# Performance work log

Hardware: AMD Instinct MI355X
Metric: run time of the kernel (lower is better)

The kernel has to match this reference:

```python
import jax, jax.numpy as jnp
import numpy as np

H, D, HID = 16, 128, 2048
B, S = 2, 2048
NUM_BLOCKS, BLOCK_SIZE = 32, 128


def _rope(x, cos, sin):
    # x: [T, H, D]; cos/sin: [T, D/2] (neox / rotate-half style)
    half = x.shape[-1] // 2
    x1, x2 = x[..., :half], x[..., half:]
    c = cos[:, None, :]
    s = sin[:, None, :]
    return jnp.concatenate([x1 * c - x2 * s, x2 * c + x1 * s], axis=-1)


def setup_inputs() -> dict:
    key = jax.random.key(0)
    ks = jax.random.split(key, 6)
    T = B * S
    hidden_states = jax.random.normal(ks[0], (T, HID), jnp.float32)
    wqkv = jax.random.normal(ks[1], (HID, 3 * HID), jnp.float32) * 0.02
    bqkv = jax.random.normal(ks[2], (3 * HID,), jnp.float32) * 0.02
    wo = jax.random.normal(ks[3], (HID, HID), jnp.float32) * 0.02
    # rotary tables, base 10000, dim = head_size
    inv_freq = 1.0 / (10000.0 ** (jnp.arange(0, D, 2, dtype=jnp.float32) / D))  # [D/2]
    pos = jnp.tile(jnp.arange(S, dtype=jnp.float32), B)  # positions per token [T]
    ang = pos[:, None] * inv_freq[None, :]  # [T, D/2]
    cos, sin = jnp.cos(ang), jnp.sin(ang)
    k_cache = jnp.zeros((NUM_BLOCKS, BLOCK_SIZE, H, D), jnp.float32)
    v_cache = jnp.zeros((NUM_BLOCKS, BLOCK_SIZE, H, D), jnp.float32)
    cu_seqlen_prefill = jnp.array([0, S, 2 * S], jnp.int32)
    slots = jnp.arange(T, dtype=jnp.int32)
    return {"hidden_states": hidden_states, "cos": cos, "sin": sin,
            "wqkv": wqkv, "bqkv": bqkv, "wo": wo,
            "k_cache": k_cache, "v_cache": v_cache,
            "cu_seqlen_prefill": cu_seqlen_prefill, "slots": slots, "max_s": S}


def reference(hidden_states, cos, sin, wqkv, bqkv, wo, k_cache, v_cache,
              cu_seqlen_prefill, slots, max_s):
    T = hidden_states.shape[0]
    # fused QKV projection (c_attn)
    qkv = hidden_states @ wqkv + bqkv  # [T, 3*H*D]
    q, k, v = jnp.split(qkv, [H * D, 2 * H * D], axis=1)
    q = q.reshape(T, H, D)
    k = k.reshape(T, H, D)
    v = v.reshape(T, H, D)
    # rotary embedding on q and k (in-place in torch; functional here)
    q = _rope(q, cos, sin)
    k = _rope(k, cos, sin)
    # reshape_and_cache: scatter post-rope k and v into paged KV cache by slot
    kc = k_cache.reshape(-1, H, D).at[slots].set(k).reshape(k_cache.shape)
    vc = v_cache.reshape(-1, H, D).at[slots].set(v).reshape(v_cache.shape)
    # prefill flash attention: varlen causal; equal-length sequences here
    b, s = T // max_s, max_s
    qb = q.reshape(b, s, H, D)
    kb = k.reshape(b, s, H, D)
    vb = v.reshape(b, s, H, D)
    scale = D ** -0.5
    scores = jnp.einsum('bqhd,bkhd->bhqk', qb, kb) * scale  # [B,H,S,S]
    causal = jnp.tril(jnp.ones((s, s), bool))
    scores = jnp.where(causal[None, None], scores, jnp.finfo(scores.dtype).min)
    probs = jax.nn.softmax(scores, axis=-1)
    attn = jnp.einsum('bhqk,bkhd->bqhd', probs, vb).reshape(T, H * D)
    out = attn @ wo  # c_proj, no bias
    return out, kc, vc
```

## Files before the change

### kernel.cpp

```cpp
#include <hip/hip_runtime.h>

using f32x4  = __attribute__((ext_vector_type(4))) float;
using frag16 = __attribute__((ext_vector_type(8))) short;
using s16x4  = __attribute__((ext_vector_type(4))) short;
using s16x8  = __attribute__((ext_vector_type(8))) short;
using u32x4  = __attribute__((ext_vector_type(4))) unsigned;

#define DI __device__ __forceinline__

constexpr int HID  = 2048;
constexpr int NH   = 16;
constexpr int HD   = 128;
constexpr int TT   = 4096;
constexpr int SEQ  = 2048;
constexpr int NQKV = 3 * HID;
constexpr float SCL = 0.08838834764831845f * 1.4426950408889634f;

DI short f2bf(float f) {
  unsigned u = __builtin_bit_cast(unsigned, f);
  unsigned r = (u + 0x7fffu + ((u >> 16) & 1u)) >> 16;
  return (short)r;
}
DI float bf2f(short s) {
  unsigned u = ((unsigned)(unsigned short)s) << 16;
  return __builtin_bit_cast(float, u);
}
DI unsigned cvtpk(float lo, float hi) {
  unsigned r;
  asm("v_cvt_pk_bf16_f32 %0, %1, %2" : "=v"(r) : "v"(lo), "v"(hi));
  return r;
}

struct alignas(8) S4h { short a, b, c, d; };

__global__ void conv_f32_bf16(const float* __restrict__ in, short* __restrict__ out) {
  int gid = blockIdx.x * 256 + threadIdx.x;
  const float4* in4 = (const float4*)in;
  float4 v = in4[gid];
  S4h o{f2bf(v.x), f2bf(v.y), f2bf(v.z), f2bf(v.w)};
  ((S4h*)out)[gid] = o;
}

template <bool IN_F32, bool PERM>
__global__ void transpose_conv(const void* __restrict__ in_, short* __restrict__ out,
                               int ldin, int R) {
  __shared__ float t[64][65];
  const float* inf = (const float*)in_;
  const short* ins = (const short*)in_;
  int tid = threadIdx.x;
  int bx = blockIdx.x, by = blockIdx.y;
#pragma unroll
  for (int i = 0; i < 4; i++) {
    int idx = i * 256 + tid;
    int r = idx >> 4, c4 = idx & 15;
    size_t gi = (size_t)(by * 64 + r) * ldin + bx * 64 + c4 * 4;
    if (IN_F32) {
      float4 v = *(const float4*)(inf + gi);
      t[r][c4 * 4] = v.x; t[r][c4 * 4 + 1] = v.y;
      t[r][c4 * 4 + 2] = v.z; t[r][c4 * 4 + 3] = v.w;
    } else {
      s16x4 v = *(const s16x4*)(ins + gi);
#pragma unroll
      for (int j = 0; j < 4; j++) t[r][c4 * 4 + j] = bf2f(v[j]);
    }
  }
  __syncthreads();
#pragma unroll
  for (int i = 0; i < 4; i++) {
    int idx = i * 256 + tid;
    int r = idx >> 4, c4 = idx & 15;
    s16x4 o;
#pragma unroll
    for (int j = 0; j < 4; j++) {
      int c = c4 * 4 + j;
      int cs = PERM ? ((c >> 5) * 32 + ((c >> 2) & 1) * 16 + ((c >> 3) & 3) * 4 + (c & 3))
                    : c;
      o[j] = f2bf(t[cs][r]);
    }
    *(s16x4*)(out + (size_t)(bx * 64 + r) * R + by * 64 + c4 * 4) = o;
  }
}

#define GLDS(src, dst)                                                     \
  __builtin_amdgcn_global_load_lds(                                        \
      (const __attribute__((address_space(1))) void*)(src),                \
      (__attribute__((address_space(3))) void*)(dst), 16, 0, 0)

template <int EPI>
__global__ __launch_bounds__(256, 2) void gemm_bt(
    const short* __restrict__ A, const short* __restrict__ Bt,
    const float* __restrict__ bias, float* __restrict__ Cout,
    const float* __restrict__ cs, const float* __restrict__ sn,
    const int* __restrict__ slots,
    short* __restrict__ Qb, short* __restrict__ Kb, short* __restrict__ Vrow,
    float* __restrict__ kc, float* __restrict__ vc,
    int M, int N, int K) {
  __shared__ alignas(16) short Al[128 * 64];
  __shared__ alignas(16) short Bl[128 * 64];
  const int tid = threadIdx.x;
  const int wid = tid >> 6, lane = tid & 63;
  const int wr = wid >> 1, wc = wid & 1;
  const int l15 = lane & 15, lg = lane >> 4;
  const int gx = gridDim.x;
  const int id = blockIdx.y * gx + blockIdx.x;
  const int nwg = gx * gridDim.y;
  const int swz = (id & 7) * (nwg >> 3) + (id >> 3);
  const int row0 = (swz / gx) * 128, col0 = (swz % gx) * 128;
  const int lr8 = lane >> 3, l7 = lane & 7;

  f32x4 acc[4][4];
#pragma unroll
  for (int i = 0; i < 4; i++)
#pragma unroll
    for (int j = 0; j < 4; j++) acc[i][j] = {0.f, 0.f, 0.f, 0.f};

  for (int kt = 0; kt < K; kt += 64) {
#pragma unroll
    for (int c = 0; c < 4; c++) {
      int chunk = c * 4 + wid;
      int r = chunk * 8 + lr8;
      int ke = (l7 * 8) ^ ((r & 7) * 8);
      GLDS(A + (size_t)(row0 + r) * K + kt + ke, Al + chunk * 512);
      GLDS(Bt + (size_t)(col0 + r) * K + kt + ke, Bl + chunk * 512);
    }
    __syncthreads();
#pragma unroll
    for (int kk = 0; kk < 2; kk++) {
      frag16 af[4], bfv[4];
#pragma unroll
      for (int ai = 0; ai < 4; ai++) {
        int r = wr * 64 + ai * 16 + l15;
        int k0 = kk * 32 + lg * 8;
        af[ai] = *(const frag16*)(Al + r * 64 + (k0 ^ ((r & 7) * 8)));
      }
#pragma unroll
      for (int bj = 0; bj < 4; bj++) {
        int r = wc * 16 + (bj & 1) * 32 + ((bj >> 1) << 6) + l15;
        int k0 = kk * 32 + lg * 8;
        bfv[bj] = *(const frag16*)(Bl + r * 64 + (k0 ^ ((r & 7) * 8)));
      }
#pragma unroll
      for (int ai = 0; ai < 4; ai++)
#pragma unroll
        for (int bj = 0; bj < 4; bj++)
          acc[ai][bj] = __builtin_amdgcn_mfma_f32_16x16x32_bf16(
              af[ai], bfv[bj], acc[ai][bj], 0, 0, 0);
    }
    __syncthreads();
  }

  if (EPI == 0) {
#pragma unroll
    for (int ai = 0; ai < 4; ai++) {
#pragma unroll
      for (int bj = 0; bj < 4; bj++) {
        int row = row0 + wr * 64 + ai * 16 + lg * 4;
        int col = col0 + wc * 16 + (bj & 1) * 32 + ((bj >> 1) << 6) + l15;
#pragma unroll
        for (int r = 0; r < 4; r++)
          Cout[(size_t)(row + r) * N + col] = acc[ai][bj][r];
      }
    }
  } else {
    const int sec = col0 >> 11;
    const int h = (col0 & 2047) >> 7;
#pragma unroll
    for (int ai = 0; ai < 4; ai++) {
#pragma unroll
      for (int bj = 0; bj < 2; bj++) {
        const int d1 = wc * 16 + bj * 32 + l15;
        const float b1 = bias[col0 + d1];
        const float b2 = bias[col0 + d1 + 64];
        const int base = h * 128 + d1;
#pragma unroll
        for (int r = 0; r < 4; r++) {
          const int tok = row0 + wr * 64 + ai * 16 + lg * 4 + r;
          float v1 = acc[ai][bj][r] + b1;
          float v2 = acc[ai][bj + 2][r] + b2;
          if (sec == 0) {
            float c = cs[tok * 64 + d1], s = sn[tok * 64 + d1];
            Qb[(size_t)tok * HID + base]      = f2bf((v1 * c - v2 * s) * SCL);
            Qb[(size_t)tok * HID + base + 64] = f2bf((v2 * c + v1 * s) * SCL);
          } else if (sec == 1) {
            float c = cs[tok * 64 + d1], s = sn[tok * 64 + d1];
            float o1 = v1 * c - v2 * s, o2 = v2 * c + v1 * s;
            int sl = slots[tok];
            Kb[(size_t)tok * HID + base]      = f2bf(o1);
            Kb[(size_t)tok * HID + base + 64] = f2bf(o2);
            kc[(size_t)sl * HID + base]      = o1;
            kc[(size_t)sl * HID + base + 64] = o2;
          } else {
            int sl = slots[tok];
            vc[(size_t)sl * HID + base]      = v1;
            vc[(size_t)sl * HID + base + 64] = v2;
            Vrow[(size_t)tok * HID + base]      = f2bf(v1);
            Vrow[(size_t)tok * HID + base + 64] = f2bf(v2);
          }
        }
      }
    }
  }
}

__global__ __launch_bounds__(256, 2) void flash_attn6(
    const short* __restrict__ Qb, const short* __restrict__ Kb,
    const short* __restrict__ Vt, short* __restrict__ attn) {
  __shared__ alignas(16) short Klds[2][64 * 128];
  __shared__ alignas(16) short Vlds[2][128 * 64];

  const int tid = threadIdx.x;
  const int w = tid >> 6, lane = tid & 63;
  const int l15 = lane & 15, lg = lane >> 4;
  const int bid = blockIdx.x;
  const int p = bid >> 5;
  const int bh = bid & 31;
  const int b = bh >> 4, h = bh & 15;

  frag16 ones;
#pragma unroll
  for (int j = 0; j < 8; j++) ones[j] = (short)0x3F80;

  auto stage = [&](int kv0, int buf) {
#pragma unroll
    for (int ci = 0; ci < 4; ci++) {
      int cc = w * 4 + ci;
      int krow = cc * 4 + (lane >> 4);
      int kss = (lane & 15) ^ (krow & 15);
      GLDS(Kb + (size_t)(b * SEQ + kv0 + krow) * HID + h * HD + kss * 8,
           Klds[buf] + cc * 512);
      int vd = cc * 8 + (lane >> 3);
      int vss = (lane & 7) ^ (vd & 7);
      GLDS(Vt + (size_t)(h * HD + vd) * TT + b * SEQ + kv0 + vss * 8,
           Vlds[buf] + cc * 512);
    }
  };

  const int qrowH = (31 - p) * 64 + w * 16;
  const int qrowL = p * 64 + w * 16;
  const int ntH = 32 - p;

  frag16 qfH[4], qfL[4];
  {
    const short* qpH = Qb + (size_t)(b * SEQ + qrowH + l15) * HID + h * HD + lg * 8;
    const short* qpL = Qb + (size_t)(b * SEQ + qrowL + l15) * HID + h * HD + lg * 8;
#pragma unroll
    for (int ds = 0; ds < 4; ds++) {
      qfH[ds] = *(const frag16*)(qpH + ds * 32);
      qfL[ds] = *(const frag16*)(qpL + ds * 32);
    }
  }
  f32x4 oH[8], oL[8];
#pragma unroll
  for (int j = 0; j < 8; j++) { oH[j] = {0.f, 0.f, 0.f, 0.f}; oL[j] = {0.f, 0.f, 0.f, 0.f}; }
  f32x4 laH = {0.f, 0.f, 0.f, 0.f}, laL = {0.f, 0.f, 0.f, 0.f};
  float mrH = -1e30f, mrL = -1e30f;

  auto proc = [&](const frag16 (&qf)[4], f32x4 (&o)[8], f32x4& la, float& mr,
                  bool diag, const short* Kl, const short* Vl) {
    f32x4 sa[4];
#pragma unroll
    for (int f = 0; f < 4; f++) sa[f] = {0.f, 0.f, 0.f, 0.f};
    __builtin_amdgcn_s_setprio(1);
#pragma unroll
    for (int ds = 0; ds < 4; ds++) {
      int phys = (ds * 4 + lg) ^ l15;
#pragma unroll
      for (int f = 0; f < 4; f++) {
        frag16 kf = *(const frag16*)(Kl + (f * 16 + l15) * 128 + phys * 8);
        sa[f] = __builtin_amdgcn_mfma_f32_16x16x32_bf16(kf, qf[ds], sa[f], 0, 0, 0);
      }
    }
    __builtin_amdgcn_s_setprio(0);
    if (diag) {
      int ql = 16 * w + l15;
#pragma unroll
      for (int f = 0; f < 4; f++)
#pragma unroll
        for (int r = 0; r < 4; r++)
          if (f * 16 + lg * 4 + r > ql) sa[f][r] = -1e30f;
    }
    float pm = sa[0][0];
#pragma unroll
    for (int f = 0; f < 4; f++)
#pragma unroll
      for (int r = 0; r < 4; r++) pm = fmaxf(pm, sa[f][r]);
    pm = fmaxf(pm, __shfl_xor(pm, 16));
    pm = fmaxf(pm, __shfl_xor(pm, 32));
    if (__any(pm > mr + 8.f)) {
      float mn = fmaxf(mr, pm);
      float frl = exp2f(mr - mn);
      mr = mn;
      float fr4[4];
#pragma unroll
      for (int r = 0; r < 4; r++)
        fr4[r] = __shfl(frl, lg * 16 + lg * 4 + r);
#pragma unroll
      for (int r = 0; r < 4; r++) {
        la[r] *= fr4[r];
#pragma unroll
        for (int j = 0; j < 8; j++) o[j][r] *= fr4[r];
      }
    }
    float pe[4][4];
#pragma unroll
    for (int f = 0; f < 4; f++)
#pragma unroll
      for (int r = 0; r < 4; r++) pe[f][r] = exp2f(sa[f][r] - mr);
    u32x4 w0, w1;
    w0[0] = cvtpk(pe[0][0], pe[0][1]); w0[1] = cvtpk(pe[0][2], pe[0][3]);
    w0[2] = cvtpk(pe[1][0], pe[1][1]); w0[3] = cvtpk(pe[1][2], pe[1][3]);
    w1[0] = cvtpk(pe[2][0], pe[2][1]); w1[1] = cvtpk(pe[2][2], pe[2][3]);
    w1[2] = cvtpk(pe[3][0], pe[3][1]); w1[3] = cvtpk(pe[3][2], pe[3][3]);
    frag16 pf0 = __builtin_bit_cast(frag16, w0);
    frag16 pf1 = __builtin_bit_cast(frag16, w1);
    __builtin_amdgcn_s_setprio(1);
    la = __builtin_amdgcn_mfma_f32_16x16x32_bf16(pf0, ones, la, 0, 0, 0);
    la = __builtin_amdgcn_mfma_f32_16x16x32_bf16(pf1, ones, la, 0, 0, 0);
#pragma unroll
    for (int j = 0; j < 8; j++) {
      int d = j * 16 + l15;
      int p0 = lg ^ (d & 7);
      int p1 = (4 + lg) ^ (d & 7);
      frag16 vf0 = *(const frag16*)(Vl + d * 64 + p0 * 8);
      frag16 vf1 = *(const frag16*)(Vl + d * 64 + p1 * 8);
      o[j] = __builtin_amdgcn_mfma_f32_16x16x32_bf16(pf0, vf0, o[j], 0, 0, 0);
      o[j] = __builtin_amdgcn_mfma_f32_16x16x32_bf16(pf1, vf1, o[j], 0, 0, 0);
    }
    __builtin_amdgcn_s_setprio(0);
  };

  stage(0, 0);
  __syncthreads();

  int cur = 0;
  for (int t = 0; t < ntH; t++) {
    if (t + 1 < ntH) stage((t + 1) * 64, cur ^ 1);
    const short* Kl = &Klds[cur][0];
    const short* Vl = &Vlds[cur][0];
    proc(qfH, oH, laH, mrH, t == ntH - 1, Kl, Vl);
    if (t <= p) proc(qfL, oL, laL, mrL, t == p, Kl, Vl);
    __syncthreads();
    cur ^= 1;
  }

  {
    float inv[4];
#pragma unroll
    for (int r = 0; r < 4; r++) inv[r] = 1.f / laH[r];
    short* op = attn + (size_t)(b * SEQ + qrowH + lg * 4) * HID + h * HD + l15;
#pragma unroll
    for (int j = 0; j < 8; j++)
#pragma unroll
      for (int r = 0; r < 4; r++)
        op[(size_t)r * HID + j * 16] = f2bf(oH[j][r] * inv[r]);
  }
  {
    float inv[4];
#pragma unroll
    for (int r = 0; r < 4; r++) inv[r] = 1.f / laL[r];
    short* op = attn + (size_t)(b * SEQ + qrowL + lg * 4) * HID + h * HD + l15;
#pragma unroll
    for (int j = 0; j < 8; j++)
#pragma unroll
      for (int r = 0; r < 4; r++)
        op[(size_t)r * HID + j * 16] = f2bf(oL[j][r] * inv[r]);
  }
}

extern "C" void kernel_launch(void* const* d_in, const int* in_sizes, int n_in,
                              void* d_out, int out_size, void* d_ws, size_t ws_size,
                              hipStream_t stream) {
  const float* hidden = (const float*)d_in[0];
  const float* cosb   = (const float*)d_in[1];
  const float* sinb   = (const float*)d_in[2];
  const float* wqkv   = (const float*)d_in[3];
  const float* bqkv   = (const float*)d_in[4];
  const float* wo     = (const float*)d_in[5];
  const int*   slots  = (const int*)d_in[9];

  float* out = (float*)d_out;
  float* kc  = out + (size_t)TT * HID;
  float* vc  = kc + (size_t)TT * HID;

  short* ws    = (short*)d_ws;
  short* Abf   = ws;
  short* Wqkvt = Abf + 8388608;
  short* Wot   = Wqkvt + 12582912;
  short* Qb    = Wot + 4194304;
  short* Kb    = Qb + 8388608;
  short* Vrow  = Kb + 8388608;
  short* Vt    = Vrow + 8388608;
  short* attnb = Abf;

  conv_f32_bf16<<<8192, 256, 0, stream>>>(hidden, Abf);
  transpose_conv<true, false><<<dim3(96, 32), 256, 0, stream>>>(wqkv, Wqkvt, NQKV, HID);
  transpose_conv<true, false><<<dim3(32, 32), 256, 0, stream>>>(wo, Wot, HID, HID);
  gemm_bt<1><<<dim3(48, 32), 256, 0, stream>>>(
      Abf, Wqkvt, bqkv, nullptr, cosb, sinb, slots, Qb, Kb, Vrow, kc, vc,
      TT, NQKV, HID);
  transpose_conv<false, true><<<dim3(32, 64), 256, 0, stream>>>(Vrow, Vt, HID, TT);
  flash_attn6<<<512, 256, 0, stream>>>(Qb, Kb, Vt, attnb);
  gemm_bt<0><<<dim3(16, 32), 256, 0, stream>>>(
      attnb, Wot, nullptr, out, nullptr, nullptr, nullptr,
      nullptr, nullptr, nullptr, nullptr, nullptr, TT, HID, HID);
}
```

Baseline: 289.2 us.

## Fuse prep kernels into one launch and deepen attention KV prefetch

Three preprocessing launches (activation conversion plus two weight transposes) are merged into a single kernel that dispatches on block index, which removes launch gaps. The flash attention loop now keeps two KV tiles in flight. It uses explicit s_waitcnt vmcnt counts and raw s_barrier instead of __syncthreads, and issues the next stage only after the buffer is released. The goal is to overlap global-to-LDS loads with compute. The hand-counted vmcnt(8) depends on exactly how many loads each stage issues, and a wrong count risks reading stale LDS data.

New measurement: 289.1 us. Within noise of the previous version (-0.1%).

```diff
diff --git a/kernel.cpp b/kernel.cpp
--- a/kernel.cpp
+++ b/kernel.cpp
@@ -33,36 +33,39 @@
 
 struct alignas(8) S4h { short a, b, c, d; };
 
-__global__ void conv_f32_bf16(const float* __restrict__ in, short* __restrict__ out) {
-  int gid = blockIdx.x * 256 + threadIdx.x;
-  const float4* in4 = (const float4*)in;
-  float4 v = in4[gid];
-  S4h o{f2bf(v.x), f2bf(v.y), f2bf(v.z), f2bf(v.w)};
-  ((S4h*)out)[gid] = o;
-}
-
-template <bool IN_F32, bool PERM>
-__global__ void transpose_conv(const void* __restrict__ in_, short* __restrict__ out,
-                               int ldin, int R) {
+__global__ void prep(const float* __restrict__ hidden, short* __restrict__ Abf,
+                     const float* __restrict__ wqkv, short* __restrict__ Wqkvt,
+                     const float* __restrict__ wo, short* __restrict__ Wot) {
   __shared__ float t[64][65];
-  const float* inf = (const float*)in_;
-  const short* ins = (const short*)in_;
-  int tid = threadIdx.x;
-  int bx = blockIdx.x, by = blockIdx.y;
+  const int bid = blockIdx.x;
+  const int tid = threadIdx.x;
+  if (bid < 8192) {
+    int gid = bid * 256 + tid;
+    float4 v = ((const float4*)hidden)[gid];
+    S4h o{f2bf(v.x), f2bf(v.y), f2bf(v.z), f2bf(v.w)};
+    ((S4h*)Abf)[gid] = o;
+    return;
+  }
+  const float* in;
+  short* out;
+  int ldin, R, bx, by;
+  if (bid < 8192 + 3072) {
+    int idx = bid - 8192;
+    in = wqkv; out = Wqkvt; ldin = NQKV; R = HID;
+    bx = idx % 96; by = idx / 96;
+  } else {
+    int idx = bid - 8192 - 3072;
+    in = wo; out = Wot; ldin = HID; R = HID;
+    bx = idx % 32; by = idx / 32;
+  }
 #pragma unroll
   for (int i = 0; i < 4; i++) {
     int idx = i * 256 + tid;
     int r = idx >> 4, c4 = idx & 15;
     size_t gi = (size_t)(by * 64 + r) * ldin + bx * 64 + c4 * 4;
-    if (IN_F32) {
-      float4 v = *(const float4*)(inf + gi);
-      t[r][c4 * 4] = v.x; t[r][c4 * 4 + 1] = v.y;
-      t[r][c4 * 4 + 2] = v.z; t[r][c4 * 4 + 3] = v.w;
-    } else {
-      s16x4 v = *(const s16x4*)(ins + gi);
-#pragma unroll
-      for (int j = 0; j < 4; j++) t[r][c4 * 4 + j] = bf2f(v[j]);
-    }
+    float4 v = *(const float4*)(in + gi);
+    t[r][c4 * 4] = v.x; t[r][c4 * 4 + 1] = v.y;
+    t[r][c4 * 4 + 2] = v.z; t[r][c4 * 4 + 3] = v.w;
   }
   __syncthreads();
 #pragma unroll
@@ -71,10 +74,35 @@
     int r = idx >> 4, c4 = idx & 15;
     s16x4 o;
 #pragma unroll
+    for (int j = 0; j < 4; j++) o[j] = f2bf(t[c4 * 4 + j][r]);
+    *(s16x4*)(out + (size_t)(bx * 64 + r) * R + by * 64 + c4 * 4) = o;
+  }
+}
+
+__global__ void transpose_perm(const short* __restrict__ in, short* __restrict__ out,
+                               int ldin, int R) {
+  __shared__ float t[64][65];
+  int tid = threadIdx.x;
+  int bx = blockIdx.x, by = blockIdx.y;
+#pragma unroll
+  for (int i = 0; i < 4; i++) {
+    int idx = i * 256 + tid;
+    int r = idx >> 4, c4 = idx & 15;
+    size_t gi = (size_t)(by * 64 + r) * ldin + bx * 64 + c4 * 4;
+    s16x4 v = *(const s16x4*)(in + gi);
+#pragma unroll
+    for (int j = 0; j < 4; j++) t[r][c4 * 4 + j] = bf2f(v[j]);
+  }
+  __syncthreads();
+#pragma unroll
+  for (int i = 0; i < 4; i++) {
+    int idx = i * 256 + tid;
+    int r = idx >> 4, c4 = idx & 15;
+    s16x4 o;
+#pragma unroll
     for (int j = 0; j < 4; j++) {
       int c = c4 * 4 + j;
-      int cs = PERM ? ((c >> 5) * 32 + ((c >> 2) & 1) * 16 + ((c >> 3) & 3) * 4 + (c & 3))
-                    : c;
+      int cs = (c >> 5) * 32 + ((c >> 2) & 1) * 16 + ((c >> 3) & 3) * 4 + (c & 3);
       o[j] = f2bf(t[cs][r]);
     }
     *(s16x4*)(out + (size_t)(bx * 64 + r) * R + by * 64 + c4 * 4) = o;
@@ -202,7 +230,7 @@
   }
 }
 
-__global__ __launch_bounds__(256, 2) void flash_attn6(
+__global__ __launch_bounds__(256, 2) void flash_attn7(
     const short* __restrict__ Qb, const short* __restrict__ Kb,
     const short* __restrict__ Vt, short* __restrict__ attn) {
   __shared__ alignas(16) short Klds[2][64 * 128];
@@ -330,16 +358,22 @@
   };
 
   stage(0, 0);
-  __syncthreads();
+  if (ntH > 1) stage(64, 1);
 
   int cur = 0;
   for (int t = 0; t < ntH; t++) {
-    if (t + 1 < ntH) stage((t + 1) * 64, cur ^ 1);
+    if (t + 1 < ntH) {
+      asm volatile("s_waitcnt vmcnt(8)" ::: "memory");
+    } else {
+      asm volatile("s_waitcnt vmcnt(0)" ::: "memory");
+    }
+    asm volatile("s_barrier" ::: "memory");
     const short* Kl = &Klds[cur][0];
     const short* Vl = &Vlds[cur][0];
     proc(qfH, oH, laH, mrH, t == ntH - 1, Kl, Vl);
     if (t <= p) proc(qfL, oL, laL, mrL, t == p, Kl, Vl);
-    __syncthreads();
+    asm volatile("s_barrier" ::: "memory");
+    if (t + 2 < ntH) stage((t + 2) * 64, cur);
     cur ^= 1;
   }
 
@@ -392,14 +426,12 @@
   short* Vt    = Vrow + 8388608;
   short* attnb = Abf;
 
-  conv_f32_bf16<<<8192, 256, 0, stream>>>(hidden, Abf);
-  transpose_conv<true, false><<<dim3(96, 32), 256, 0, stream>>>(wqkv, Wqkvt, NQKV, HID);
-  transpose_conv<true, false><<<dim3(32, 32), 256, 0, stream>>>(wo, Wot, HID, HID);
+  prep<<<8192 + 3072 + 1024, 256, 0, stream>>>(hidden, Abf, wqkv, Wqkvt, wo, Wot);
   gemm_bt<1><<<dim3(48, 32), 256, 0, stream>>>(
       Abf, Wqkvt, bqkv, nullptr, cosb, sinb, slots, Qb, Kb, Vrow, kc, vc,
       TT, NQKV, HID);
-  transpose_conv<false, true><<<dim3(32, 64), 256, 0, stream>>>(Vrow, Vt, HID, TT);
-  flash_attn6<<<512, 256, 0, stream>>>(Qb, Kb, Vt, attnb);
+  transpose_perm<<<dim3(32, 64), 256, 0, stream>>>(Vrow, Vt, HID, TT);
+  flash_attn7<<<512, 256, 0, stream>>>(Qb, Kb, Vt, attnb);
   gemm_bt<0><<<dim3(16, 32), 256, 0, stream>>>(
       attnb, Wot, nullptr, out, nullptr, nullptr, nullptr,
       nullptr, nullptr, nullptr, nullptr, nullptr, TT, HID, HID);
```
